# Performance work log

Hardware: AMD Instinct MI355X
Metric: run time of the kernel (lower is better)

Reference implementation:

```python
import jax, jax.numpy as jnp
import numpy as np

SPARSITY_RATIO = 0.5

def setup_inputs() -> dict:
    key = jax.random.key(0)
    x = jax.random.normal(key, (32, 128, 128, 128), dtype=jnp.float32)
    return {"x": x}

def reference(x) -> jnp.ndarray:
    B, C, H, W = x.shape
    k = int(SPARSITY_RATIO * H * W)
    absx = jnp.abs(x)
    flat = absx.reshape(B, C, H * W)
    # k-th largest |x| per (b, c) is the threshold
    topvals = jax.lax.top_k(flat, k)[0]          # [B, C, k]
    thresh = topvals[:, :, -1][:, :, None, None]  # [B, C, 1, 1]
    comp = (absx >= thresh).astype(x.dtype)
    return comp * x
```

## Files before the change

### kernel.cpp

```cpp
#include <hip/hip_runtime.h>

#define THREADS 512
#define HW 16384
#define K_SEL 8192u
#define NB1 2048
#define NB2 1024
#define NB3 1024
#define VPT 8

static_assert(THREADS * VPT * 4 == HW, "row tiling");

typedef unsigned uint32x4 __attribute__((ext_vector_type(4)));

template <int NBINS>
__device__ __forceinline__ void find_bin_wave0(const unsigned* __restrict__ hist,
                                               unsigned kRem, unsigned* __restrict__ bc) {
  constexpr int bpl = NBINS >> 6;
  const int lane = (int)(threadIdx.x & 63);
  const int base = lane * bpl;
  unsigned s = 0;
#pragma unroll
  for (int j = 0; j < bpl; ++j) s += hist[base + ((j + lane) & (bpl - 1))];
  unsigned suf = s;
#pragma unroll
  for (int off = 1; off < 64; off <<= 1) {
    unsigned w = __shfl_down(suf, off);
    if (lane + off < 64) suf += w;
  }
  const unsigned cumAbove = suf - s;
  const bool hit = (cumAbove < kRem) && (kRem <= suf);
  const unsigned long long m = __ballot(hit);
  const int tl = (int)__builtin_ctzll(m);
  const unsigned cumTl = __shfl(cumAbove, tl);
  const int j = lane & (bpl - 1);
  const unsigned h = hist[tl * bpl + j];
  unsigned sufc = h;
#pragma unroll
  for (int off = 1; off < 32; off <<= 1) {
    if (off < bpl) {
      unsigned w = __shfl_down(sufc, off);
      if (j + off < bpl) sufc += w;
    }
  }
  const unsigned cumW = sufc - h;
  const bool hit2 = ((cumTl + cumW) < kRem) && (kRem <= cumTl + cumW + h);
  const unsigned long long m2 = __ballot(hit2);
  const int jl = (int)__builtin_ctzll(m2) & (bpl - 1);
  const unsigned kw = __shfl(cumW, jl);
  if (lane == 0) {
    bc[0] = (unsigned)(tl * bpl + jl);
    bc[1] = kRem - cumTl - kw;
  }
}

extern "C" __global__ __launch_bounds__(THREADS, 8)
void sparsify_topk_kernel(const float* __restrict__ x, float* __restrict__ out) {
  __shared__ unsigned h1[NB1];
  __shared__ unsigned h2[NB2];
  __shared__ unsigned h3[NB3];
  __shared__ unsigned bc[2];

  const int t = (int)threadIdx.x;
  const size_t rowOff = (size_t)blockIdx.x * (HW / 4);
  const uint4*    src = (const uint4*)x + rowOff;
  uint32x4*       dst = (uint32x4*)out + rowOff;

  uint4 v[VPT];
#pragma unroll
  for (int i = 0; i < VPT; ++i) v[i] = src[i * THREADS + t];

#pragma unroll
  for (int i = 0; i < NB1 / THREADS; ++i) h1[t + i * THREADS] = 0;
#pragma unroll
  for (int i = 0; i < NB2 / THREADS; ++i) h2[t + i * THREADS] = 0;
#pragma unroll
  for (int i = 0; i < NB3 / THREADS; ++i) h3[t + i * THREADS] = 0;
  __syncthreads();

#pragma unroll
  for (int i = 0; i < VPT; ++i) {
    atomicAdd(&h1[(v[i].x & 0x7fffffffu) >> 20], 1u);
    atomicAdd(&h1[(v[i].y & 0x7fffffffu) >> 20], 1u);
    atomicAdd(&h1[(v[i].z & 0x7fffffffu) >> 20], 1u);
    atomicAdd(&h1[(v[i].w & 0x7fffffffu) >> 20], 1u);
  }
  __syncthreads();
  if (t < 64) find_bin_wave0<NB1>(h1, K_SEL, bc);
  __syncthreads();
  const unsigned T1 = bc[0];
  unsigned kRem = bc[1];

#pragma unroll
  for (int i = 0; i < VPT; ++i) {
    unsigned a;
    a = v[i].x & 0x7fffffffu; if ((a >> 20) == T1) atomicAdd(&h2[(a >> 10) & (NB2 - 1)], 1u);
    a = v[i].y & 0x7fffffffu; if ((a >> 20) == T1) atomicAdd(&h2[(a >> 10) & (NB2 - 1)], 1u);
    a = v[i].z & 0x7fffffffu; if ((a >> 20) == T1) atomicAdd(&h2[(a >> 10) & (NB2 - 1)], 1u);
    a = v[i].w & 0x7fffffffu; if ((a >> 20) == T1) atomicAdd(&h2[(a >> 10) & (NB2 - 1)], 1u);
  }
  __syncthreads();
  if (t < 64) find_bin_wave0<NB2>(h2, kRem, bc);
  __syncthreads();
  const unsigned pref2 = (T1 << 10) | bc[0];
  kRem = bc[1];

#pragma unroll
  for (int i = 0; i < VPT; ++i) {
    unsigned a;
    a = v[i].x & 0x7fffffffu; if ((a >> 10) == pref2) atomicAdd(&h3[a & (NB3 - 1)], 1u);
    a = v[i].y & 0x7fffffffu; if ((a >> 10) == pref2) atomicAdd(&h3[a & (NB3 - 1)], 1u);
    a = v[i].z & 0x7fffffffu; if ((a >> 10) == pref2) atomicAdd(&h3[a & (NB3 - 1)], 1u);
    a = v[i].w & 0x7fffffffu; if ((a >> 10) == pref2) atomicAdd(&h3[a & (NB3 - 1)], 1u);
  }
  __syncthreads();
  if (t < 64) find_bin_wave0<NB3>(h3, kRem, bc);
  __syncthreads();
  const unsigned thr = (pref2 << 10) | bc[0];

#pragma unroll
  for (int i = 0; i < VPT; ++i) {
    uint32x4 w;
    w.x = v[i].x; w.y = v[i].y; w.z = v[i].z; w.w = v[i].w;
    w.x = ((w.x & 0x7fffffffu) >= thr) ? w.x : 0u;
    w.y = ((w.y & 0x7fffffffu) >= thr) ? w.y : 0u;
    w.z = ((w.z & 0x7fffffffu) >= thr) ? w.z : 0u;
    w.w = ((w.w & 0x7fffffffu) >= thr) ? w.w : 0u;
    __builtin_nontemporal_store(w, &dst[i * THREADS + t]);
  }
}

extern "C" void kernel_launch(void* const* d_in, const int* in_sizes, int n_in,
                              void* d_out, int out_size, void* d_ws, size_t ws_size,
                              hipStream_t stream) {
  (void)n_in; (void)d_ws; (void)ws_size; (void)out_size;
  const float* x = (const float*)d_in[0];
  float* out = (float*)d_out;
  const int rows = in_sizes[0] / HW;
  sparsify_topk_kernel<<<dim3(rows), dim3(THREADS), 0, stream>>>(x, out);
}
```

Measured before the change: 96.91 us.

## Compact threshold-bin candidates into shared list and write output speculatively

Values are no longer held in registers across all passes. Each row is read twice from global memory. The second pass writes the output early, keeping every element above the first-level bin, and records the candidates that fall in the threshold bin into a shared-memory list. The third histogram and the final fix-up then work only on that short list, using scattered stores, with a full re-read fallback if the list overflows. This is meant to cut register pressure and the third full pass. The cost is an extra global read of the row, doubled LDS use per block, and scattered writes.

New measurement: 133.3 us. 1.38x slower.

```diff
diff --git a/kernel.cpp b/kernel.cpp
--- a/kernel.cpp
+++ b/kernel.cpp
@@ -7,6 +7,7 @@
 #define NB2 1024
 #define NB3 1024
 #define VPT 8
+#define CAP 2048
 
 static_assert(THREADS * VPT * 4 == HW, "row tiling");
 
@@ -58,16 +59,16 @@
   __shared__ unsigned h1[NB1];
   __shared__ unsigned h2[NB2];
   __shared__ unsigned h3[NB3];
+  __shared__ unsigned listIdx[CAP];
+  __shared__ unsigned listVal[CAP];
   __shared__ unsigned bc[2];
+  __shared__ unsigned cnt;
 
   const int t = (int)threadIdx.x;
   const size_t rowOff = (size_t)blockIdx.x * (HW / 4);
-  const uint4*    src = (const uint4*)x + rowOff;
-  uint32x4*       dst = (uint32x4*)out + rowOff;
-
-  uint4 v[VPT];
-#pragma unroll
-  for (int i = 0; i < VPT; ++i) v[i] = src[i * THREADS + t];
+  const uint4*    src  = (const uint4*)x + rowOff;
+  uint32x4*       dst  = (uint32x4*)out + rowOff;
+  unsigned*       dstS = (unsigned*)dst;
 
 #pragma unroll
   for (int i = 0; i < NB1 / THREADS; ++i) h1[t + i * THREADS] = 0;
@@ -75,57 +76,87 @@
   for (int i = 0; i < NB2 / THREADS; ++i) h2[t + i * THREADS] = 0;
 #pragma unroll
   for (int i = 0; i < NB3 / THREADS; ++i) h3[t + i * THREADS] = 0;
+  if (t == 0) cnt = 0;
   __syncthreads();
 
 #pragma unroll
   for (int i = 0; i < VPT; ++i) {
-    atomicAdd(&h1[(v[i].x & 0x7fffffffu) >> 20], 1u);
-    atomicAdd(&h1[(v[i].y & 0x7fffffffu) >> 20], 1u);
-    atomicAdd(&h1[(v[i].z & 0x7fffffffu) >> 20], 1u);
-    atomicAdd(&h1[(v[i].w & 0x7fffffffu) >> 20], 1u);
+    const uint4 u = src[i * THREADS + t];
+    atomicAdd(&h1[(u.x & 0x7fffffffu) >> 20], 1u);
+    atomicAdd(&h1[(u.y & 0x7fffffffu) >> 20], 1u);
+    atomicAdd(&h1[(u.z & 0x7fffffffu) >> 20], 1u);
+    atomicAdd(&h1[(u.w & 0x7fffffffu) >> 20], 1u);
   }
   __syncthreads();
   if (t < 64) find_bin_wave0<NB1>(h1, K_SEL, bc);
   __syncthreads();
   const unsigned T1 = bc[0];
   unsigned kRem = bc[1];
+  const unsigned keepMin1 = (T1 + 1u) << 20;
 
 #pragma unroll
   for (int i = 0; i < VPT; ++i) {
+    const uint4 u = src[i * THREADS + t];
+    const unsigned eIdx = (unsigned)((i * THREADS + t) * 4);
+    uint32x4 w;
     unsigned a;
-    a = v[i].x & 0x7fffffffu; if ((a >> 20) == T1) atomicAdd(&h2[(a >> 10) & (NB2 - 1)], 1u);
-    a = v[i].y & 0x7fffffffu; if ((a >> 20) == T1) atomicAdd(&h2[(a >> 10) & (NB2 - 1)], 1u);
-    a = v[i].z & 0x7fffffffu; if ((a >> 20) == T1) atomicAdd(&h2[(a >> 10) & (NB2 - 1)], 1u);
-    a = v[i].w & 0x7fffffffu; if ((a >> 20) == T1) atomicAdd(&h2[(a >> 10) & (NB2 - 1)], 1u);
+#define P2_ONE(comp, o)                                                     \
+    a = u.comp & 0x7fffffffu;                                               \
+    w.comp = (a >= keepMin1) ? u.comp : 0u;                                 \
+    if ((a >> 20) == T1) {                                                  \
+      atomicAdd(&h2[(a >> 10) & (NB2 - 1)], 1u);                            \
+      const unsigned p = atomicAdd(&cnt, 1u);                               \
+      if (p < CAP) { listIdx[p] = eIdx + o; listVal[p] = u.comp; }          \
+    }
+    P2_ONE(x, 0) P2_ONE(y, 1) P2_ONE(z, 2) P2_ONE(w, 3)
+#undef P2_ONE
+    __builtin_nontemporal_store(w, &dst[i * THREADS + t]);
   }
   __syncthreads();
   if (t < 64) find_bin_wave0<NB2>(h2, kRem, bc);
   __syncthreads();
   const unsigned pref2 = (T1 << 10) | bc[0];
   kRem = bc[1];
+  const unsigned nC = cnt;
+  const bool fallback = (nC > CAP);
 
+  if (!fallback) {
+    for (unsigned i = t; i < nC; i += THREADS) {
+      const unsigned a = listVal[i] & 0x7fffffffu;
+      if ((a >> 10) == pref2) atomicAdd(&h3[a & (NB3 - 1)], 1u);
+    }
+  } else {
 #pragma unroll
-  for (int i = 0; i < VPT; ++i) {
-    unsigned a;
-    a = v[i].x & 0x7fffffffu; if ((a >> 10) == pref2) atomicAdd(&h3[a & (NB3 - 1)], 1u);
-    a = v[i].y & 0x7fffffffu; if ((a >> 10) == pref2) atomicAdd(&h3[a & (NB3 - 1)], 1u);
-    a = v[i].z & 0x7fffffffu; if ((a >> 10) == pref2) atomicAdd(&h3[a & (NB3 - 1)], 1u);
-    a = v[i].w & 0x7fffffffu; if ((a >> 10) == pref2) atomicAdd(&h3[a & (NB3 - 1)], 1u);
+    for (int i = 0; i < VPT; ++i) {
+      const uint4 u = src[i * THREADS + t];
+      unsigned a;
+      a = u.x & 0x7fffffffu; if ((a >> 10) == pref2) atomicAdd(&h3[a & (NB3 - 1)], 1u);
+      a = u.y & 0x7fffffffu; if ((a >> 10) == pref2) atomicAdd(&h3[a & (NB3 - 1)], 1u);
+      a = u.z & 0x7fffffffu; if ((a >> 10) == pref2) atomicAdd(&h3[a & (NB3 - 1)], 1u);
+      a = u.w & 0x7fffffffu; if ((a >> 10) == pref2) atomicAdd(&h3[a & (NB3 - 1)], 1u);
+    }
   }
   __syncthreads();
   if (t < 64) find_bin_wave0<NB3>(h3, kRem, bc);
   __syncthreads();
   const unsigned thr = (pref2 << 10) | bc[0];
 
+  if (!fallback) {
+    for (unsigned i = t; i < nC; i += THREADS) {
+      const unsigned raw = listVal[i];
+      if ((raw & 0x7fffffffu) >= thr) dstS[listIdx[i]] = raw;
+    }
+  } else {
 #pragma unroll
-  for (int i = 0; i < VPT; ++i) {
-    uint32x4 w;
-    w.x = v[i].x; w.y = v[i].y; w.z = v[i].z; w.w = v[i].w;
-    w.x = ((w.x & 0x7fffffffu) >= thr) ? w.x : 0u;
-    w.y = ((w.y & 0x7fffffffu) >= thr) ? w.y : 0u;
-    w.z = ((w.z & 0x7fffffffu) >= thr) ? w.z : 0u;
-    w.w = ((w.w & 0x7fffffffu) >= thr) ? w.w : 0u;
-    __builtin_nontemporal_store(w, &dst[i * THREADS + t]);
+    for (int i = 0; i < VPT; ++i) {
+      const uint4 u = src[i * THREADS + t];
+      uint32x4 w;
+      w.x = ((u.x & 0x7fffffffu) >= thr) ? u.x : 0u;
+      w.y = ((u.y & 0x7fffffffu) >= thr) ? u.y : 0u;
+      w.z = ((u.z & 0x7fffffffu) >= thr) ? u.z : 0u;
+      w.w = ((u.w & 0x7fffffffu) >= thr) ? u.w : 0u;
+      __builtin_nontemporal_store(w, &dst[i * THREADS + t]);
+    }
   }
 }
 
```
